# Optimization experiments

Measured on AMD Instinct MI355X. Metric: run time of the kernel, lower is better.

## Reference

```python
import jax, jax.numpy as jnp
import numpy as np

B, S, HIDDEN = 2, 2048, 2048
N_HEADS, N_KV_HEADS = 32, 8
HEAD_DIM = HIDDEN // N_HEADS          # 64
HALF = HEAD_DIM // 2                  # 32
N_REP = N_HEADS // N_KV_HEADS         # 4
NEG_INF = -1e9


def setup_inputs() -> dict:
    key = jax.random.key(0)
    ks = jax.random.split(key, 5)
    scale = 0.02
    x = jax.random.normal(ks[0], (B, S, HIDDEN), dtype=jnp.float32)
    wq = jax.random.normal(ks[1], (HIDDEN, N_HEADS * HEAD_DIM), dtype=jnp.float32) * scale
    wk = jax.random.normal(ks[2], (HIDDEN, N_KV_HEADS * HEAD_DIM), dtype=jnp.float32) * scale
    wv = jax.random.normal(ks[3], (HIDDEN, N_KV_HEADS * HEAD_DIM), dtype=jnp.float32) * scale
    wo = jax.random.normal(ks[4], (HIDDEN, HIDDEN), dtype=jnp.float32) * scale
    # Llama rotary frequencies: theta = 10000^{-2i/d}, angles = pos * theta
    inv_freq = 1.0 / (10000.0 ** (np.arange(0, HEAD_DIM, 2, dtype=np.float32) / HEAD_DIM))
    angles = np.arange(S, dtype=np.float32)[:, None] * inv_freq[None, :]  # [S, HALF]
    freqs_cos = jnp.asarray(np.cos(angles), dtype=jnp.float32)
    freqs_sin = jnp.asarray(np.sin(angles), dtype=jnp.float32)
    mask = jnp.tril(jnp.ones((S, S), dtype=bool))[None, None]  # causal [1,1,S,S]
    return {"x": x, "wq": wq, "wk": wk, "wv": wv, "wo": wo,
            "freqs_cos": freqs_cos, "freqs_sin": freqs_sin, "mask": mask}


def _apply_rope(t, cos, sin):
    # t: [B, S, H, HEAD_DIM]; cos/sin: [S, HALF] -> broadcast [1, S, 1, HALF]
    tr, ti = t[..., ::2], t[..., 1::2]           # real/imag halves (interleaved pairing)
    c = cos[None, :, None, :]
    s = sin[None, :, None, :]
    out_r = tr * c - ti * s
    out_i = tr * s + ti * c
    out = jnp.stack([out_r, out_i], axis=-1)     # [B,S,H,HALF,2]
    return out.reshape(t.shape)                  # re-interleave


def reference(x, wq, wk, wv, wo, freqs_cos, freqs_sin, mask):
    b, s, _ = x.shape
    xq = (x @ wq).reshape(b, s, N_HEADS, HEAD_DIM)
    xk = (x @ wk).reshape(b, s, N_KV_HEADS, HEAD_DIM)
    xv = (x @ wv).reshape(b, s, N_KV_HEADS, HEAD_DIM)
    xq = _apply_rope(xq, freqs_cos, freqs_sin)
    xk = _apply_rope(xk, freqs_cos, freqs_sin)
    # repeat_kv: interleave-repeat kv heads to match query heads
    xk = jnp.repeat(xk, N_REP, axis=2)           # [B,S,N_HEADS,HEAD_DIM]
    xv = jnp.repeat(xv, N_REP, axis=2)
    q = jnp.transpose(xq, (0, 2, 1, 3))          # [B,H,S,D]
    k = jnp.transpose(xk, (0, 2, 1, 3))
    v = jnp.transpose(xv, (0, 2, 1, 3))
    attn = jnp.einsum('bhqd,bhkd->bhqk', q, k) / jnp.sqrt(jnp.float32(HEAD_DIM))
    attn = attn + (1.0 - mask.astype(attn.dtype)) * NEG_INF  # keras Softmax masking
    attn = jax.nn.softmax(attn, axis=-1)
    out = jnp.einsum('bhqk,bhkd->bhqd', attn, v)
    out = jnp.transpose(out, (0, 2, 1, 3)).reshape(b, s, HIDDEN)
    return out @ wo
```

## Files before the change

### kernel.cpp

```cpp
#include <hip/hip_runtime.h>
#include <cstdint>
#include <cstddef>

#define S_LEN 2048
#define HIDDEN 2048
#define NH 32
#define NKV 8
#define HD 64
#define QKV_W 3072

typedef __bf16 bf16;
typedef __bf16 bf16x8 __attribute__((ext_vector_type(8)));
typedef __bf16 bf16x4 __attribute__((ext_vector_type(4)));
typedef float f32x4 __attribute__((ext_vector_type(4)));

__device__ __forceinline__ void async16(const bf16* g, bf16* l) {
  __builtin_amdgcn_global_load_lds((const __attribute__((address_space(1))) void*)g,
                                   (__attribute__((address_space(3))) void*)l, 16, 0, 0);
}

__global__ void cast_x_kernel(const float* __restrict__ in, bf16* __restrict__ out, int n4) {
  int i = blockIdx.x * blockDim.x + threadIdx.x;
  if (i >= n4) return;
  f32x4 v = ((const f32x4*)in)[i];
  bf16x4 o;
  o[0] = (bf16)v[0]; o[1] = (bf16)v[1]; o[2] = (bf16)v[2]; o[3] = (bf16)v[3];
  ((bf16x4*)out)[i] = o;
}

__global__ void transpose_cast_kernel(const float* __restrict__ in, bf16* __restrict__ out,
                                      int K, int N) {
  __shared__ float tile[32][33];
  const int n0 = blockIdx.x * 32, k0 = blockIdx.y * 32;
  const int tx = threadIdx.x, ty = threadIdx.y;
#pragma unroll
  for (int i = 0; i < 32; i += 8)
    tile[ty + i][tx] = in[(size_t)(k0 + ty + i) * N + n0 + tx];
  __syncthreads();
#pragma unroll
  for (int i = 0; i < 32; i += 8)
    out[(size_t)(n0 + ty + i) * K + k0 + tx] = (bf16)tile[tx][ty + i];
}

__global__ void vt_kernel(const bf16* __restrict__ qkv, bf16* __restrict__ vt) {
  __shared__ bf16 tile[32][33];
  const int s0 = blockIdx.x * 32, c0 = blockIdx.y * 32, b = blockIdx.z;
  const int tx = threadIdx.x, ty = threadIdx.y;
#pragma unroll
  for (int i = 0; i < 32; i += 8)
    tile[ty + i][tx] = qkv[((size_t)b * S_LEN + s0 + ty + i) * QKV_W + 2560 + c0 + tx];
  __syncthreads();
#pragma unroll
  for (int i = 0; i < 32; i += 8)
    vt[((size_t)b * 512 + c0 + ty + i) * S_LEN + s0 + tx] = tile[tx][ty + i];
}

template <int OUT_BF16>
__global__ __launch_bounds__(256) void gemm_bt_kernel(const bf16* __restrict__ A,
                                                      const bf16* __restrict__ Bt,
                                                      void* __restrict__ Cv,
                                                      int M, int N, int K) {
  __shared__ bf16 Al[128 * 32];
  __shared__ bf16 Bl[128 * 32];
  const int tid = threadIdx.x;
  const int lane = tid & 63, w = tid >> 6;
  const int quad = lane >> 4, l16 = lane & 15;
  const int m0 = blockIdx.y * 128, n0 = blockIdx.x * 128;
  const int wm = (w >> 1) * 64, wn = (w & 1) * 64;
  f32x4 acc[4][4] = {};
  const int srow = tid >> 2, scol = (tid & 3) * 8;
  const bf16* Ar0 = A + (size_t)(m0 + srow) * K + scol;
  const bf16* Ar1 = A + (size_t)(m0 + 64 + srow) * K + scol;
  const bf16* Br0 = Bt + (size_t)(n0 + srow) * K + scol;
  const bf16* Br1 = Bt + (size_t)(n0 + 64 + srow) * K + scol;
  bf16* al0 = Al + tid * 8;
  bf16* al1 = Al + 2048 + tid * 8;
  bf16* bl0 = Bl + tid * 8;
  bf16* bl1 = Bl + 2048 + tid * 8;
  for (int kt = 0; kt < K; kt += 32) {
    __syncthreads();
    async16(Ar0 + kt, al0);
    async16(Ar1 + kt, al1);
    async16(Br0 + kt, bl0);
    async16(Br1 + kt, bl1);
    __syncthreads();
    bf16x8 a[4], b[4];
#pragma unroll
    for (int mi = 0; mi < 4; ++mi)
      a[mi] = *(const bf16x8*)(Al + (wm + mi * 16 + l16) * 32 + quad * 8);
#pragma unroll
    for (int ni = 0; ni < 4; ++ni)
      b[ni] = *(const bf16x8*)(Bl + (wn + ni * 16 + l16) * 32 + quad * 8);
#pragma unroll
    for (int mi = 0; mi < 4; ++mi)
#pragma unroll
      for (int ni = 0; ni < 4; ++ni)
        acc[mi][ni] = __builtin_amdgcn_mfma_f32_16x16x32_bf16(a[mi], b[ni], acc[mi][ni], 0, 0, 0);
  }
#pragma unroll
  for (int mi = 0; mi < 4; ++mi)
#pragma unroll
    for (int ni = 0; ni < 4; ++ni)
#pragma unroll
      for (int i = 0; i < 4; ++i) {
        const int row = m0 + wm + mi * 16 + quad * 4 + i;
        const int col = n0 + wn + ni * 16 + l16;
        if (OUT_BF16)
          ((bf16*)Cv)[(size_t)row * N + col] = (bf16)acc[mi][ni][i];
        else
          ((float*)Cv)[(size_t)row * N + col] = acc[mi][ni][i];
      }
}

__global__ void rope_kernel(bf16* __restrict__ qkv, const float* __restrict__ cosp,
                            const float* __restrict__ sinp, int total) {
  int idx = blockIdx.x * blockDim.x + threadIdx.x;
  if (idx >= total) return;
  const int row = idx / 320;
  const int col = (idx - row * 320) * 8;
  const int s = row & (S_LEN - 1);
  const int j0 = (col >> 1) & 31;
  bf16* ptr = qkv + (size_t)row * QKV_W + col;
  bf16x8 v = *(bf16x8*)ptr;
#pragma unroll
  for (int u = 0; u < 4; ++u) {
    const float tr = (float)v[2 * u], ti = (float)v[2 * u + 1];
    const float c = cosp[s * 32 + j0 + u], sn = sinp[s * 32 + j0 + u];
    v[2 * u] = (bf16)(tr * c - ti * sn);
    v[2 * u + 1] = (bf16)(tr * sn + ti * c);
  }
  *(bf16x8*)ptr = v;
}

__global__ __launch_bounds__(256) void attn_kernel(const bf16* __restrict__ qkv,
                                                   const bf16* __restrict__ vt,
                                                   bf16* __restrict__ out) {
  __shared__ bf16 Kl[64][72];
  __shared__ bf16 Vl[64][72];
  __shared__ bf16 Pl[4][16][72];
  const int tid = threadIdx.x;
  const int lane = tid & 63, w = tid >> 6;
  const int quad = lane >> 4, l16 = lane & 15;
  const int gx = blockIdx.x, h = blockIdx.y, b = blockIdx.z;
  const int kvh = h >> 2;
  const bf16* Qbase = qkv + ((size_t)b * S_LEN) * QKV_W + h * HD;
  const bf16* Kbase = qkv + ((size_t)b * S_LEN) * QKV_W + 2048 + kvh * HD;
  const bf16* Vtb = vt + ((size_t)b * 512 + kvh * 64) * S_LEN;
  const int srow = tid >> 3, scol = (tid & 7) * 8;

  for (int pass = 0; pass < 2; ++pass) {
    const int qt = pass ? (31 - gx) : gx;
    const int q0 = qt * 64;
    const int qrow = q0 + w * 16 + l16;
    const bf16x8 aq0 = *(const bf16x8*)(Qbase + (size_t)qrow * QKV_W + quad * 8);
    const bf16x8 aq1 = *(const bf16x8*)(Qbase + (size_t)qrow * QKV_W + 32 + quad * 8);
    float l[4] = {0.f, 0.f, 0.f, 0.f};
    f32x4 o[4] = {};

    for (int t = 0; t <= qt; ++t) {
      const int kt = t * 64;
      __syncthreads();
      *(bf16x8*)&Kl[srow][scol]      = *(const bf16x8*)(Kbase + (size_t)(kt + srow) * QKV_W + scol);
      *(bf16x8*)&Kl[srow + 32][scol] = *(const bf16x8*)(Kbase + (size_t)(kt + srow + 32) * QKV_W + scol);
      *(bf16x8*)&Vl[srow][scol]      = *(const bf16x8*)(Vtb + (size_t)srow * S_LEN + kt + scol);
      *(bf16x8*)&Vl[srow + 32][scol] = *(const bf16x8*)(Vtb + (size_t)(srow + 32) * S_LEN + kt + scol);
      __syncthreads();
      f32x4 c[4] = {};
#pragma unroll
      for (int j = 0; j < 4; ++j) {
        const bf16x8 bk0 = *(const bf16x8*)&Kl[j * 16 + l16][quad * 8];
        const bf16x8 bk1 = *(const bf16x8*)&Kl[j * 16 + l16][32 + quad * 8];
        c[j] = __builtin_amdgcn_mfma_f32_16x16x32_bf16(aq0, bk0, c[j], 0, 0, 0);
        c[j] = __builtin_amdgcn_mfma_f32_16x16x32_bf16(aq1, bk1, c[j], 0, 0, 0);
      }
      const bool diag = (t == qt);
#pragma unroll
      for (int i = 0; i < 4; ++i) {
        const int r = w * 16 + quad * 4 + i;
        float p[4];
#pragma unroll
        for (int j = 0; j < 4; ++j) {
          p[j] = __expf(fmaf(c[j][i], 0.125f, -4.0f));
          if (diag && (j * 16 + l16 > r)) p[j] = 0.f;
        }
        l[i] += (p[0] + p[1]) + (p[2] + p[3]);
#pragma unroll
        for (int j = 0; j < 4; ++j) Pl[w][quad * 4 + i][j * 16 + l16] = (bf16)p[j];
      }
      const bf16x8 ap0 = *(const bf16x8*)&Pl[w][l16][quad * 8];
      const bf16x8 ap1 = *(const bf16x8*)&Pl[w][l16][32 + quad * 8];
#pragma unroll
      for (int dt = 0; dt < 4; ++dt) {
        const bf16x8 bv0 = *(const bf16x8*)&Vl[dt * 16 + l16][quad * 8];
        const bf16x8 bv1 = *(const bf16x8*)&Vl[dt * 16 + l16][32 + quad * 8];
        o[dt] = __builtin_amdgcn_mfma_f32_16x16x32_bf16(ap0, bv0, o[dt], 0, 0, 0);
        o[dt] = __builtin_amdgcn_mfma_f32_16x16x32_bf16(ap1, bv1, o[dt], 0, 0, 0);
      }
    }
#pragma unroll
    for (int i = 0; i < 4; ++i) {
      float li = l[i];
      li += __shfl_xor(li, 1);
      li += __shfl_xor(li, 2);
      li += __shfl_xor(li, 4);
      li += __shfl_xor(li, 8);
      const float rl = 1.0f / li;
      const int r = q0 + w * 16 + quad * 4 + i;
#pragma unroll
      for (int dt = 0; dt < 4; ++dt)
        out[((size_t)b * S_LEN + r) * HIDDEN + h * HD + dt * 16 + l16] = (bf16)(o[dt][i] * rl);
    }
  }
}

extern "C" void kernel_launch(void* const* d_in, const int* in_sizes, int n_in,
                              void* d_out, int out_size, void* d_ws, size_t ws_size,
                              hipStream_t stream) {
  const float* x = (const float*)d_in[0];
  const float* wq = (const float*)d_in[1];
  const float* wk = (const float*)d_in[2];
  const float* wv = (const float*)d_in[3];
  const float* wo = (const float*)d_in[4];
  const float* fc = (const float*)d_in[5];
  const float* fs = (const float*)d_in[6];

  char* ws = (char*)d_ws;
  bf16* xb   = (bf16*)(ws);
  bf16* wT   = (bf16*)(ws + 16777216);
  bf16* woT  = (bf16*)(ws + 29360128);
  bf16* qkv  = (bf16*)(ws + 37748736);
  bf16* aout = (bf16*)(ws + 62914560);
  bf16* vt   = xb;

  cast_x_kernel<<<8192, 256, 0, stream>>>(x, xb, 2097152);
  transpose_cast_kernel<<<dim3(64, 64), dim3(32, 8), 0, stream>>>(wq, wT, 2048, 2048);
  transpose_cast_kernel<<<dim3(16, 64), dim3(32, 8), 0, stream>>>(wk, wT + (size_t)2048 * 2048, 2048, 512);
  transpose_cast_kernel<<<dim3(16, 64), dim3(32, 8), 0, stream>>>(wv, wT + (size_t)2560 * 2048, 2048, 512);
  transpose_cast_kernel<<<dim3(64, 64), dim3(32, 8), 0, stream>>>(wo, woT, 2048, 2048);

  gemm_bt_kernel<1><<<dim3(24, 32), 256, 0, stream>>>(xb, wT, (void*)qkv, 4096, 3072, 2048);
  rope_kernel<<<5120, 256, 0, stream>>>(qkv, fc, fs, 1310720);
  vt_kernel<<<dim3(64, 16, 2), dim3(32, 8), 0, stream>>>(qkv, vt);
  attn_kernel<<<dim3(16, 32, 2), 256, 0, stream>>>(qkv, vt, aout);
  gemm_bt_kernel<0><<<dim3(16, 32), 256, 0, stream>>>(aout, woT, d_out, 4096, 2048, 2048);
}
```

Baseline: 362.3 us.

## Fuse RoPE and V-transpose into QKV GEMM epilogue; use 32x32 MFMA attention

The QKV GEMM epilogue now applies rotary embedding to the Q/K columns and writes V directly in transposed layout. This removes the separate rope and vt kernels and their extra passes over memory. The attention kernel is restructured to use 32x32x16 MFMA tiles with 128-query blocks per workgroup, each wave handling 32 queries, and skips fully masked tiles per wave. In exchange the epilogue gains shuffles and scattered cos/sin loads, and workgroup count halves, which lowers parallelism.

```diff
diff --git a/kernel.cpp b/kernel.cpp
--- a/kernel.cpp
+++ b/kernel.cpp
@@ -13,6 +13,7 @@
 typedef __bf16 bf16x8 __attribute__((ext_vector_type(8)));
 typedef __bf16 bf16x4 __attribute__((ext_vector_type(4)));
 typedef float f32x4 __attribute__((ext_vector_type(4)));
+typedef float f32x16 __attribute__((ext_vector_type(16)));
 
 __device__ __forceinline__ void async16(const bf16* g, bf16* l) {
   __builtin_amdgcn_global_load_lds((const __attribute__((address_space(1))) void*)g,
@@ -42,24 +43,14 @@
     out[(size_t)(n0 + ty + i) * K + k0 + tx] = (bf16)tile[tx][ty + i];
 }
 
-__global__ void vt_kernel(const bf16* __restrict__ qkv, bf16* __restrict__ vt) {
-  __shared__ bf16 tile[32][33];
-  const int s0 = blockIdx.x * 32, c0 = blockIdx.y * 32, b = blockIdx.z;
-  const int tx = threadIdx.x, ty = threadIdx.y;
-#pragma unroll
-  for (int i = 0; i < 32; i += 8)
-    tile[ty + i][tx] = qkv[((size_t)b * S_LEN + s0 + ty + i) * QKV_W + 2560 + c0 + tx];
-  __syncthreads();
-#pragma unroll
-  for (int i = 0; i < 32; i += 8)
-    vt[((size_t)b * 512 + c0 + ty + i) * S_LEN + s0 + tx] = tile[tx][ty + i];
-}
-
-template <int OUT_BF16>
+template <int MODE>
 __global__ __launch_bounds__(256) void gemm_bt_kernel(const bf16* __restrict__ A,
                                                       const bf16* __restrict__ Bt,
                                                       void* __restrict__ Cv,
-                                                      int M, int N, int K) {
+                                                      int M, int N, int K,
+                                                      const float* __restrict__ cosp,
+                                                      const float* __restrict__ sinp,
+                                                      bf16* __restrict__ vtp) {
   __shared__ bf16 Al[128 * 32];
   __shared__ bf16 Bl[128 * 32];
   const int tid = threadIdx.x;
@@ -97,118 +88,138 @@
       for (int ni = 0; ni < 4; ++ni)
         acc[mi][ni] = __builtin_amdgcn_mfma_f32_16x16x32_bf16(a[mi], b[ni], acc[mi][ni], 0, 0, 0);
   }
-#pragma unroll
-  for (int mi = 0; mi < 4; ++mi)
-#pragma unroll
-    for (int ni = 0; ni < 4; ++ni)
-#pragma unroll
-      for (int i = 0; i < 4; ++i) {
-        const int row = m0 + wm + mi * 16 + quad * 4 + i;
+  if (MODE == 0) {
+#pragma unroll
+    for (int mi = 0; mi < 4; ++mi)
+#pragma unroll
+      for (int ni = 0; ni < 4; ++ni)
+#pragma unroll
+        for (int i = 0; i < 4; ++i) {
+          const int row = m0 + wm + mi * 16 + quad * 4 + i;
+          const int col = n0 + wn + ni * 16 + l16;
+          ((float*)Cv)[(size_t)row * N + col] = acc[mi][ni][i];
+        }
+  } else if (n0 < 2560) {
+#pragma unroll
+    for (int mi = 0; mi < 4; ++mi)
+#pragma unroll
+      for (int ni = 0; ni < 4; ++ni)
+#pragma unroll
+        for (int i = 0; i < 4; ++i) {
+          const int row = m0 + wm + mi * 16 + quad * 4 + i;
+          const int col = n0 + wn + ni * 16 + l16;
+          const float v = acc[mi][ni][i];
+          const float p = __shfl_xor(v, 1);
+          const int st = row & (S_LEN - 1);
+          const int j = (col & 63) >> 1;
+          const float cc = cosp[st * 32 + j], ss = sinp[st * 32 + j];
+          const float ov = (l16 & 1) ? (p * ss + v * cc) : (v * cc - p * ss);
+          ((bf16*)Cv)[(size_t)row * N + col] = (bf16)ov;
+        }
+  } else {
+#pragma unroll
+    for (int mi = 0; mi < 4; ++mi)
+#pragma unroll
+      for (int ni = 0; ni < 4; ++ni) {
         const int col = n0 + wn + ni * 16 + l16;
-        if (OUT_BF16)
-          ((bf16*)Cv)[(size_t)row * N + col] = (bf16)acc[mi][ni][i];
-        else
-          ((float*)Cv)[(size_t)row * N + col] = acc[mi][ni][i];
-      }
-}
-
-__global__ void rope_kernel(bf16* __restrict__ qkv, const float* __restrict__ cosp,
-                            const float* __restrict__ sinp, int total) {
-  int idx = blockIdx.x * blockDim.x + threadIdx.x;
-  if (idx >= total) return;
-  const int row = idx / 320;
-  const int col = (idx - row * 320) * 8;
-  const int s = row & (S_LEN - 1);
-  const int j0 = (col >> 1) & 31;
-  bf16* ptr = qkv + (size_t)row * QKV_W + col;
-  bf16x8 v = *(bf16x8*)ptr;
-#pragma unroll
-  for (int u = 0; u < 4; ++u) {
-    const float tr = (float)v[2 * u], ti = (float)v[2 * u + 1];
-    const float c = cosp[s * 32 + j0 + u], sn = sinp[s * 32 + j0 + u];
-    v[2 * u] = (bf16)(tr * c - ti * sn);
-    v[2 * u + 1] = (bf16)(tr * sn + ti * c);
+        const int c = col - 2560;
+        const int row0 = m0 + wm + mi * 16 + quad * 4;
+        const int batch = row0 >> 11, st0 = row0 & (S_LEN - 1);
+        bf16x4 d4;
+#pragma unroll
+        for (int i = 0; i < 4; ++i) d4[i] = (bf16)acc[mi][ni][i];
+        *(bf16x4*)&vtp[((size_t)batch * 512 + c) * S_LEN + st0] = d4;
+      }
   }
-  *(bf16x8*)ptr = v;
 }
 
 __global__ __launch_bounds__(256) void attn_kernel(const bf16* __restrict__ qkv,
                                                    const bf16* __restrict__ vt,
                                                    bf16* __restrict__ out) {
-  __shared__ bf16 Kl[64][72];
-  __shared__ bf16 Vl[64][72];
-  __shared__ bf16 Pl[4][16][72];
+  __shared__ bf16 Kl[64 * 72];
+  __shared__ bf16 Vl[64 * 72];
+  __shared__ bf16 Pl[4][32 * 72];
   const int tid = threadIdx.x;
   const int lane = tid & 63, w = tid >> 6;
-  const int quad = lane >> 4, l16 = lane & 15;
+  const int l32 = lane & 31, half = lane >> 5;
   const int gx = blockIdx.x, h = blockIdx.y, b = blockIdx.z;
   const int kvh = h >> 2;
-  const bf16* Qbase = qkv + ((size_t)b * S_LEN) * QKV_W + h * HD;
   const bf16* Kbase = qkv + ((size_t)b * S_LEN) * QKV_W + 2048 + kvh * HD;
-  const bf16* Vtb = vt + ((size_t)b * 512 + kvh * 64) * S_LEN;
-  const int srow = tid >> 3, scol = (tid & 7) * 8;
+  const bf16* vtb = vt + ((size_t)b * 512 + kvh * 64) * S_LEN;
+  const int sr = tid >> 3, sc = (tid & 7) * 8;
+  bf16* pw = Pl[w];
 
   for (int pass = 0; pass < 2; ++pass) {
-    const int qt = pass ? (31 - gx) : gx;
-    const int q0 = qt * 64;
-    const int qrow = q0 + w * 16 + l16;
-    const bf16x8 aq0 = *(const bf16x8*)(Qbase + (size_t)qrow * QKV_W + quad * 8);
-    const bf16x8 aq1 = *(const bf16x8*)(Qbase + (size_t)qrow * QKV_W + 32 + quad * 8);
-    float l[4] = {0.f, 0.f, 0.f, 0.f};
-    f32x4 o[4] = {};
-
-    for (int t = 0; t <= qt; ++t) {
+    const int qt = pass ? (15 - gx) : gx;
+    const int Q0 = qt * 128;
+    const int qw = Q0 + w * 32;
+    const int q = qw + l32;
+    const bf16* Qrow = qkv + ((size_t)b * S_LEN + q) * QKV_W + h * HD;
+    bf16x8 bq[4];
+#pragma unroll
+    for (int dc = 0; dc < 4; ++dc) bq[dc] = *(const bf16x8*)(Qrow + dc * 16 + half * 8);
+    float l_acc = 0.f;
+    f32x16 o0 = {}, o1 = {};
+    const int ntiles = 2 * qt + 2;
+    for (int t = 0; t < ntiles; ++t) {
       const int kt = t * 64;
       __syncthreads();
-      *(bf16x8*)&Kl[srow][scol]      = *(const bf16x8*)(Kbase + (size_t)(kt + srow) * QKV_W + scol);
-      *(bf16x8*)&Kl[srow + 32][scol] = *(const bf16x8*)(Kbase + (size_t)(kt + srow + 32) * QKV_W + scol);
-      *(bf16x8*)&Vl[srow][scol]      = *(const bf16x8*)(Vtb + (size_t)srow * S_LEN + kt + scol);
-      *(bf16x8*)&Vl[srow + 32][scol] = *(const bf16x8*)(Vtb + (size_t)(srow + 32) * S_LEN + kt + scol);
+      *(bf16x8*)&Kl[sr * 72 + sc]        = *(const bf16x8*)(Kbase + (size_t)(kt + sr) * QKV_W + sc);
+      *(bf16x8*)&Kl[(sr + 32) * 72 + sc] = *(const bf16x8*)(Kbase + (size_t)(kt + sr + 32) * QKV_W + sc);
+      *(bf16x8*)&Vl[sr * 72 + sc]        = *(const bf16x8*)(vtb + (size_t)sr * S_LEN + kt + sc);
+      *(bf16x8*)&Vl[(sr + 32) * 72 + sc] = *(const bf16x8*)(vtb + (size_t)(sr + 32) * S_LEN + kt + sc);
       __syncthreads();
-      f32x4 c[4] = {};
-#pragma unroll
-      for (int j = 0; j < 4; ++j) {
-        const bf16x8 bk0 = *(const bf16x8*)&Kl[j * 16 + l16][quad * 8];
-        const bf16x8 bk1 = *(const bf16x8*)&Kl[j * 16 + l16][32 + quad * 8];
-        c[j] = __builtin_amdgcn_mfma_f32_16x16x32_bf16(aq0, bk0, c[j], 0, 0, 0);
-        c[j] = __builtin_amdgcn_mfma_f32_16x16x32_bf16(aq1, bk1, c[j], 0, 0, 0);
-      }
-      const bool diag = (t == qt);
-#pragma unroll
-      for (int i = 0; i < 4; ++i) {
-        const int r = w * 16 + quad * 4 + i;
-        float p[4];
-#pragma unroll
-        for (int j = 0; j < 4; ++j) {
-          p[j] = __expf(fmaf(c[j][i], 0.125f, -4.0f));
-          if (diag && (j * 16 + l16 > r)) p[j] = 0.f;
+      if (kt > qw + 31) continue;
+      f32x16 s0 = {}, s1 = {};
+#pragma unroll
+      for (int dc = 0; dc < 4; ++dc) {
+        const bf16x8 ak0 = *(const bf16x8*)&Kl[l32 * 72 + dc * 16 + half * 8];
+        const bf16x8 ak1 = *(const bf16x8*)&Kl[(32 + l32) * 72 + dc * 16 + half * 8];
+        s0 = __builtin_amdgcn_mfma_f32_32x32x16_bf16(ak0, bq[dc], s0, 0, 0, 0);
+        s1 = __builtin_amdgcn_mfma_f32_32x32x16_bf16(ak1, bq[dc], s1, 0, 0, 0);
+      }
+      const bool needMask = (kt + 63 > qw);
+#pragma unroll
+      for (int ks = 0; ks < 2; ++ks) {
+        const f32x16 sv = ks ? s1 : s0;
+#pragma unroll
+        for (int r = 0; r < 4; ++r) {
+          bf16x4 pv;
+#pragma unroll
+          for (int c = 0; c < 4; ++c) {
+            float p = __expf(fmaf(sv[r * 4 + c], 0.125f, -4.0f));
+            const int key = kt + ks * 32 + 8 * r + 4 * half + c;
+            if (needMask && key > q) p = 0.f;
+            l_acc += p;
+            pv[c] = (bf16)p;
+          }
+          *(bf16x4*)&pw[l32 * 72 + ks * 32 + 8 * r + 4 * half] = pv;
         }
-        l[i] += (p[0] + p[1]) + (p[2] + p[3]);
-#pragma unroll
-        for (int j = 0; j < 4; ++j) Pl[w][quad * 4 + i][j * 16 + l16] = (bf16)p[j];
-      }
-      const bf16x8 ap0 = *(const bf16x8*)&Pl[w][l16][quad * 8];
-      const bf16x8 ap1 = *(const bf16x8*)&Pl[w][l16][32 + quad * 8];
-#pragma unroll
-      for (int dt = 0; dt < 4; ++dt) {
-        const bf16x8 bv0 = *(const bf16x8*)&Vl[dt * 16 + l16][quad * 8];
-        const bf16x8 bv1 = *(const bf16x8*)&Vl[dt * 16 + l16][32 + quad * 8];
-        o[dt] = __builtin_amdgcn_mfma_f32_16x16x32_bf16(ap0, bv0, o[dt], 0, 0, 0);
-        o[dt] = __builtin_amdgcn_mfma_f32_16x16x32_bf16(ap1, bv1, o[dt], 0, 0, 0);
+      }
+      bf16x8 bp[4];
+#pragma unroll
+      for (int kc = 0; kc < 4; ++kc) bp[kc] = *(const bf16x8*)&pw[l32 * 72 + kc * 16 + half * 8];
+#pragma unroll
+      for (int kc = 0; kc < 4; ++kc) {
+        const bf16x8 av0 = *(const bf16x8*)&Vl[l32 * 72 + kc * 16 + half * 8];
+        const bf16x8 av1 = *(const bf16x8*)&Vl[(32 + l32) * 72 + kc * 16 + half * 8];
+        o0 = __builtin_amdgcn_mfma_f32_32x32x16_bf16(av0, bp[kc], o0, 0, 0, 0);
+        o1 = __builtin_amdgcn_mfma_f32_32x32x16_bf16(av1, bp[kc], o1, 0, 0, 0);
       }
     }
-#pragma unroll
-    for (int i = 0; i < 4; ++i) {
-      float li = l[i];
-      li += __shfl_xor(li, 1);
-      li += __shfl_xor(li, 2);
-      li += __shfl_xor(li, 4);
-      li += __shfl_xor(li, 8);
-      const float rl = 1.0f / li;
-      const int r = q0 + w * 16 + quad * 4 + i;
-#pragma unroll
-      for (int dt = 0; dt < 4; ++dt)
-        out[((size_t)b * S_LEN + r) * HIDDEN + h * HD + dt * 16 + l16] = (bf16)(o[dt][i] * rl);
+    const float lt = l_acc + __shfl_xor(l_acc, 32);
+    const float rl = 1.0f / lt;
+    bf16* orow = out + ((size_t)b * S_LEN + q) * HIDDEN + h * HD;
+#pragma unroll
+    for (int dsub = 0; dsub < 2; ++dsub) {
+      const f32x16 ov = dsub ? o1 : o0;
+#pragma unroll
+      for (int r = 0; r < 4; ++r) {
+        bf16x4 d4;
+#pragma unroll
+        for (int c = 0; c < 4; ++c) d4[c] = (bf16)(ov[r * 4 + c] * rl);
+        *(bf16x4*)(orow + dsub * 32 + 8 * r + 4 * half) = d4;
+      }
     }
   }
 }
@@ -230,7 +241,7 @@
   bf16* woT  = (bf16*)(ws + 29360128);
   bf16* qkv  = (bf16*)(ws + 37748736);
   bf16* aout = (bf16*)(ws + 62914560);
-  bf16* vt   = xb;
+  bf16* vt   = (bf16*)(ws + 79691776);
 
   cast_x_kernel<<<8192, 256, 0, stream>>>(x, xb, 2097152);
   transpose_cast_kernel<<<dim3(64, 64), dim3(32, 8), 0, stream>>>(wq, wT, 2048, 2048);
@@ -238,9 +249,7 @@
   transpose_cast_kernel<<<dim3(16, 64), dim3(32, 8), 0, stream>>>(wv, wT + (size_t)2560 * 2048, 2048, 512);
   transpose_cast_kernel<<<dim3(64, 64), dim3(32, 8), 0, stream>>>(wo, woT, 2048, 2048);
 
-  gemm_bt_kernel<1><<<dim3(24, 32), 256, 0, stream>>>(xb, wT, (void*)qkv, 4096, 3072, 2048);
-  rope_kernel<<<5120, 256, 0, stream>>>(qkv, fc, fs, 1310720);
-  vt_kernel<<<dim3(64, 16, 2), dim3(32, 8), 0, stream>>>(qkv, vt);
-  attn_kernel<<<dim3(16, 32, 2), 256, 0, stream>>>(qkv, vt, aout);
-  gemm_bt_kernel<0><<<dim3(16, 32), 256, 0, stream>>>(aout, woT, d_out, 4096, 2048, 2048);
-}
+  gemm_bt_kernel<1><<<dim3(24, 32), 256, 0, stream>>>(xb, wT, (void*)qkv, 4096, 3072, 2048, fc, fs, vt);
+  attn_kernel<<<dim3(8, 32, 2), 256, 0, stream>>>(qkv, vt, aout);
+  gemm_bt_kernel<0><<<dim3(16, 32), 256, 0, stream>>>(aout, woT, d_out, 4096, 2048, 2048, nullptr, nullptr, nullptr);
+}
```

Result: slower. 371.0 us (+2.4%).
